# Performance work log

Measured on AMD Instinct MI355X. Metric: run time of the kernel, lower is better.

The kernel has to match this reference:

```python
import jax, jax.numpy as jnp
import numpy as np

ODIM = 8192      # output dim (slice target)
MSIZE = 64       # tile size
N_BLOCKS = 1024  # size of shared block bank


def setup_inputs() -> dict:
    key = jax.random.key(0)
    k1, k2, k3, k4 = jax.random.split(key, 4)
    x = jax.random.normal(k1, (256, 8192), dtype=jnp.float32)
    # bank of msize x msize module blocks (scaled like fan-in init)
    blocks = jax.random.normal(k2, (N_BLOCKS, MSIZE, MSIZE), dtype=jnp.float32) * 0.02
    bound = 1.0 / np.sqrt(ODIM).astype(np.float32)
    bias = jax.random.uniform(k3, (ODIM,), dtype=jnp.float32, minval=-bound, maxval=bound)
    # parts: [icount, ocount] indices into the block bank
    parts = jax.random.randint(k4, (128, 128), 0, N_BLOCKS)
    return {"x": x, "blocks": blocks, "bias": bias, "parts": parts}


def reference(x, blocks, bias, parts):
    icount, ocount = parts.shape
    m = blocks.shape[-1]
    # build_mosaic: gather blocks per parts and tile into a dense weight matrix
    fc = blocks[parts]                                   # [ic, oc, m, m]
    fc_mat = fc.transpose(0, 2, 1, 3).reshape(icount * m, ocount * m)
    # idim (8192) is divisible by msize, so pad is identity (rem == 0 branch)
    y = x @ fc_mat                                       # [B, oc*m]
    y = y[..., :ODIM] + bias                             # slice + bias; post = Identity
    return y
```

## Files before the change

### kernel.cpp

```cpp
#include <hip/hip_runtime.h>
#include <stdint.h>

#define BATCH 256
#define IDIM  8192
#define ODIM  8192
#define MS    64
#define IC    128
#define OC    128
#define NB    1024

#define TM 256
#define TN 256
#define KSPLIT 8
#define NIB (IC / KSPLIT)

typedef __bf16 bf16x8 __attribute__((ext_vector_type(8)));
typedef float  floatx4 __attribute__((ext_vector_type(4)));

#define WAITCNT_VM(n) ((((n) & 15) | (((n) >> 4) << 14)) | 0x70 | 0xF00)

__device__ __forceinline__ void async_load16(unsigned short* lds_p, const unsigned short* g_p) {
    __builtin_amdgcn_global_load_lds(
        (const __attribute__((address_space(1))) unsigned int*)g_p,
        (__attribute__((address_space(3))) unsigned int*)lds_p,
        16, 0, 0);
}

__device__ __forceinline__ unsigned short f32_to_bf16(float f) {
    unsigned int u = __float_as_uint(f);
    u += 0x7FFFu + ((u >> 16) & 1u);
    return (unsigned short)(u >> 16);
}

#define XCONV_BLKS 1024
#define PT_BLKS 64
__global__ void k_convert(const float* __restrict__ x, const float* __restrict__ blocks,
                          const int* __restrict__ parts,
                          unsigned short* __restrict__ xb, unsigned short* __restrict__ bt,
                          int* __restrict__ pT) {
    __shared__ float tile[MS][MS + 1];
    int b = blockIdx.x;
    if (b < NB) {
        const float4* src4 = (const float4*)(blocks + (size_t)b * MS * MS);
        unsigned short* dst = bt + (size_t)b * MS * MS;
        #pragma unroll
        for (int i = 0; i < 4; ++i) {
            int slot = i * 256 + threadIdx.x;
            int r = slot >> 4, c4 = (slot & 15) * 4;
            float4 v = src4[slot];
            tile[r][c4 + 0] = v.x; tile[r][c4 + 1] = v.y;
            tile[r][c4 + 2] = v.z; tile[r][c4 + 3] = v.w;
        }
        __syncthreads();
        #pragma unroll
        for (int i = 0; i < 2; ++i) {
            int slot = i * 256 + threadIdx.x;
            int c = slot >> 3, o = slot & 7;
            union { unsigned short s[8]; uint4 v; } u;
            #pragma unroll
            for (int j = 0; j < 8; ++j) u.s[j] = f32_to_bf16(tile[o * 8 + j][c]);
            *(uint4*)(dst + c * MS + o * 8) = u.v;
        }
    } else if (b < NB + XCONV_BLKS) {
        int t = (b - NB) * 256 + threadIdx.x;
        const float4* x4 = (const float4*)x;
        float4 a = x4[2 * t], bb = x4[2 * t + 1];
        union { unsigned short s[8]; uint4 v; } u;
        u.s[0] = f32_to_bf16(a.x);  u.s[1] = f32_to_bf16(a.y);
        u.s[2] = f32_to_bf16(a.z);  u.s[3] = f32_to_bf16(a.w);
        u.s[4] = f32_to_bf16(bb.x); u.s[5] = f32_to_bf16(bb.y);
        u.s[6] = f32_to_bf16(bb.z); u.s[7] = f32_to_bf16(bb.w);
        ((uint4*)xb)[t] = u.v;
    } else {
        int t = (b - NB - XCONV_BLKS) * 256 + threadIdx.x;
        int oc = t >> 7, ic = t & 127;
        pT[t] = parts[ic * OC + oc];
    }
}

__global__ __launch_bounds__(1024, 1)
void k_mosaic_gemm(const unsigned short* __restrict__ xb,
                   const unsigned short* __restrict__ bt,
                   const int* __restrict__ pT,
                   float* __restrict__ partial) {
    __shared__ __align__(16) unsigned short a_lds[2][TM * MS];
    __shared__ __align__(16) unsigned short b_lds[2][TN * MS];

    const int tid  = threadIdx.x;
    const int lane = tid & 63;
    const int wave = tid >> 6;
    const int wrow = wave >> 2;
    const int wcol = wave & 3;
    const int nt = blockIdx.x;
    const int ks = blockIdx.y;

    const int ob0 = nt * 4;
    const int ib0 = ks * NIB;

    const int row  = lane & 15;
    const int quad = lane >> 4;

    int pv = pT[(ob0 + (lane >> 4)) * IC + ib0 + (lane & 15)];

    int a_off[2][4], b_off[2][4];
    #pragma unroll
    for (int kk = 0; kk < 2; ++kk) {
        int oct = kk * 4 + quad;
        #pragma unroll
        for (int mi = 0; mi < 4; ++mi) {
            int r = wrow * 64 + mi * 16 + row;
            a_off[kk][mi] = r * MS + ((oct ^ (r & 7)) << 3);
        }
        #pragma unroll
        for (int ni = 0; ni < 4; ++ni) {
            int n = wcol * 64 + ni * 16 + row;
            b_off[kk][ni] = n * MS + ((oct ^ (n & 7)) << 3);
        }
    }

    floatx4 acc[4][4];
    #pragma unroll
    for (int mi = 0; mi < 4; ++mi)
        #pragma unroll
        for (int ni = 0; ni < 4; ++ni)
            acc[mi][ni] = (floatx4){0.f, 0.f, 0.f, 0.f};

#define STAGE(buf, ib_, q0, q1, q2, q3) do {                                  \
    _Pragma("unroll")                                                         \
    for (int j = 0; j < 2; ++j) {                                             \
        int slot = j * 1024 + tid;                                            \
        int m = slot >> 3;                                                    \
        int oct = (slot & 7) ^ (m & 7);                                       \
        async_load16(&a_lds[buf][slot * 8],                                   \
                     xb + (size_t)m * IDIM + (ib_) * MS + oct * 8);           \
    }                                                                         \
    _Pragma("unroll")                                                         \
    for (int j = 0; j < 2; ++j) {                                             \
        int slot = j * 1024 + tid;                                            \
        int n = slot >> 3;                                                    \
        int oct = (slot & 7) ^ (n & 7);                                       \
        int p = (j == 0) ? ((tid < 512) ? (q0) : (q1))                        \
                         : ((tid < 512) ? (q2) : (q3));                       \
        async_load16(&b_lds[buf][slot * 8],                                   \
                     bt + (size_t)p * (MS * MS) + (n & 63) * MS + oct * 8);   \
    } } while (0)

#define COMPUTE(buf) do {                                                     \
    _Pragma("unroll")                                                         \
    for (int kk = 0; kk < 2; ++kk) {                                          \
        bf16x8 af[4], bfr[4];                                                 \
        _Pragma("unroll")                                                     \
        for (int mi = 0; mi < 4; ++mi)                                        \
            af[mi] = *(const bf16x8*)&a_lds[buf][a_off[kk][mi]];              \
        _Pragma("unroll")                                                     \
        for (int ni = 0; ni < 4; ++ni)                                        \
            bfr[ni] = *(const bf16x8*)&b_lds[buf][b_off[kk][ni]];             \
        _Pragma("unroll")                                                     \
        for (int mi = 0; mi < 4; ++mi)                                        \
            _Pragma("unroll")                                                 \
            for (int ni = 0; ni < 4; ++ni)                                    \
                acc[mi][ni] = __builtin_amdgcn_mfma_f32_16x16x32_bf16(        \
                    af[mi], bfr[ni], acc[mi][ni], 0, 0, 0);                   \
    } } while (0)

    {
        int q0 = __shfl(pv, 0), q1 = __shfl(pv, 16), q2 = __shfl(pv, 32), q3 = __shfl(pv, 48);
        STAGE(0, ib0 + 0, q0, q1, q2, q3);
    }

    for (int i = 0; i < NIB - 1; ++i) {
        int q0 = __shfl(pv, i + 1),      q1 = __shfl(pv, 16 + i + 1);
        int q2 = __shfl(pv, 32 + i + 1), q3 = __shfl(pv, 48 + i + 1);
        STAGE((i + 1) & 1, ib0 + i + 1, q0, q1, q2, q3);
        __builtin_amdgcn_s_waitcnt(WAITCNT_VM(4));
        __builtin_amdgcn_s_barrier();
        COMPUTE(i & 1);
        __builtin_amdgcn_s_barrier();
    }
    __builtin_amdgcn_s_waitcnt(WAITCNT_VM(0));
    __builtin_amdgcn_s_barrier();
    COMPUTE((NIB - 1) & 1);

    float* out = partial + (size_t)ks * BATCH * ODIM;
    #pragma unroll
    for (int mi = 0; mi < 4; ++mi)
        #pragma unroll
        for (int ni = 0; ni < 4; ++ni)
            #pragma unroll
            for (int r = 0; r < 4; ++r) {
                int rowg = wrow * 64 + mi * 16 + quad * 4 + r;
                int colg = nt * TN + wcol * 64 + ni * 16 + row;
                out[(size_t)rowg * ODIM + colg] = acc[mi][ni][r];
            }
}

__global__ void k_reduce_bias(const float* __restrict__ partial,
                              const float* __restrict__ bias,
                              float* __restrict__ out) {
    int t = blockIdx.x * 256 + threadIdx.x;
    const float4* b4 = (const float4*)bias;
    float4 c = b4[t & (ODIM / 4 - 1)];
    float4 r = {c.x, c.y, c.z, c.w};
    #pragma unroll
    for (int k = 0; k < KSPLIT; ++k) {
        const float4* p = (const float4*)(partial + (size_t)k * BATCH * ODIM);
        float4 a = p[t];
        r.x += a.x; r.y += a.y; r.z += a.z; r.w += a.w;
    }
    ((float4*)out)[t] = r;
}

extern "C" void kernel_launch(void* const* d_in, const int* in_sizes, int n_in,
                              void* d_out, int out_size, void* d_ws, size_t ws_size,
                              hipStream_t stream) {
    const float* x      = (const float*)d_in[0];
    const float* blocks = (const float*)d_in[1];
    const float* bias   = (const float*)d_in[2];
    const int*   parts  = (const int*)d_in[3];
    float* out = (float*)d_out;

    char* ws = (char*)d_ws;
    unsigned short* xb      = (unsigned short*)ws;
    unsigned short* btb     = (unsigned short*)(ws + (4u << 20));
    int*            pTr     = (int*)(ws + (12u << 20));
    float*          partial = (float*)(ws + (13u << 20));

    k_convert<<<NB + XCONV_BLKS + PT_BLKS, 256, 0, stream>>>(x, blocks, parts, xb, btb, pTr);
    k_mosaic_gemm<<<dim3(ODIM / TN, KSPLIT), 1024, 0, stream>>>(xb, btb, pTr, partial);
    k_reduce_bias<<<(BATCH * ODIM) / (256 * 4), 256, 0, stream>>>(partial, bias, out);
}
```

Baseline: 125.5 us.

## Switch GEMM to 256x128 tiles with triple-buffered LDS and split-K of four

After: 118.9 us. 1.06x faster.

```diff
diff --git a/kernel.cpp b/kernel.cpp
--- a/kernel.cpp
+++ b/kernel.cpp
@@ -10,9 +10,12 @@
 #define NB    1024
 
 #define TM 256
-#define TN 256
-#define KSPLIT 8
+#define TN 128
+#define KSPLIT 4
 #define NIB (IC / KSPLIT)
+
+#define STAGE_USH (48 * 1024 / 2)
+#define B_OFF_USH (32 * 1024 / 2)
 
 typedef __bf16 bf16x8 __attribute__((ext_vector_type(8)));
 typedef float  floatx4 __attribute__((ext_vector_type(4)));
@@ -78,29 +81,29 @@
     }
 }
 
-__global__ __launch_bounds__(1024, 1)
+extern __shared__ unsigned short smem[];
+
+__global__ __launch_bounds__(512, 1)
 void k_mosaic_gemm(const unsigned short* __restrict__ xb,
                    const unsigned short* __restrict__ bt,
                    const int* __restrict__ pT,
                    float* __restrict__ partial) {
-    __shared__ __align__(16) unsigned short a_lds[2][TM * MS];
-    __shared__ __align__(16) unsigned short b_lds[2][TN * MS];
-
     const int tid  = threadIdx.x;
     const int lane = tid & 63;
     const int wave = tid >> 6;
-    const int wrow = wave >> 2;
-    const int wcol = wave & 3;
+    const int wrow = wave >> 1;
+    const int wcol = wave & 1;
     const int nt = blockIdx.x;
     const int ks = blockIdx.y;
 
-    const int ob0 = nt * 4;
+    const int ob0 = nt * 2;
     const int ib0 = ks * NIB;
 
     const int row  = lane & 15;
     const int quad = lane >> 4;
 
-    int pv = pT[(ob0 + (lane >> 4)) * IC + ib0 + (lane & 15)];
+    int pv0 = pT[ob0 * IC + ib0 + (lane & 31)];
+    int pv1 = pT[(ob0 + 1) * IC + ib0 + (lane & 31)];
 
     int a_off[2][4], b_off[2][4];
     #pragma unroll
@@ -114,7 +117,7 @@
         #pragma unroll
         for (int ni = 0; ni < 4; ++ni) {
             int n = wcol * 64 + ni * 16 + row;
-            b_off[kk][ni] = n * MS + ((oct ^ (n & 7)) << 3);
+            b_off[kk][ni] = B_OFF_USH + n * MS + ((oct ^ (n & 7)) << 3);
         }
     }
 
@@ -125,36 +128,35 @@
         for (int ni = 0; ni < 4; ++ni)
             acc[mi][ni] = (floatx4){0.f, 0.f, 0.f, 0.f};
 
-#define STAGE(buf, ib_, q0, q1, q2, q3) do {                                  \
+#define STAGE(base, ib_, p0_, p1_) do {                                       \
     _Pragma("unroll")                                                         \
-    for (int j = 0; j < 2; ++j) {                                             \
-        int slot = j * 1024 + tid;                                            \
+    for (int j = 0; j < 4; ++j) {                                             \
+        int slot = j * 512 + tid;               \
         int m = slot >> 3;                                                    \
         int oct = (slot & 7) ^ (m & 7);                                       \
-        async_load16(&a_lds[buf][slot * 8],                                   \
+        async_load16(smem + (base) + slot * 8,                                \
                      xb + (size_t)m * IDIM + (ib_) * MS + oct * 8);           \
     }                                                                         \
     _Pragma("unroll")                                                         \
     for (int j = 0; j < 2; ++j) {                                             \
-        int slot = j * 1024 + tid;                                            \
+        int slot = j * 512 + tid;               \
         int n = slot >> 3;                                                    \
         int oct = (slot & 7) ^ (n & 7);                                       \
-        int p = (j == 0) ? ((tid < 512) ? (q0) : (q1))                        \
-                         : ((tid < 512) ? (q2) : (q3));                       \
-        async_load16(&b_lds[buf][slot * 8],                                   \
+        int p = (j == 0) ? (p0_) : (p1_);                                     \
+        async_load16(smem + (base) + B_OFF_USH + slot * 8,                    \
                      bt + (size_t)p * (MS * MS) + (n & 63) * MS + oct * 8);   \
     } } while (0)
 
-#define COMPUTE(buf) do {                                                     \
+#define COMPUTE(base) do {                                                    \
     _Pragma("unroll")                                                         \
     for (int kk = 0; kk < 2; ++kk) {                                          \
         bf16x8 af[4], bfr[4];                                                 \
         _Pragma("unroll")                                                     \
         for (int mi = 0; mi < 4; ++mi)                                        \
-            af[mi] = *(const bf16x8*)&a_lds[buf][a_off[kk][mi]];              \
+            af[mi] = *(const bf16x8*)(smem + (base) + a_off[kk][mi]);         \
         _Pragma("unroll")                                                     \
         for (int ni = 0; ni < 4; ++ni)                                        \
-            bfr[ni] = *(const bf16x8*)&b_lds[buf][b_off[kk][ni]];             \
+            bfr[ni] = *(const bf16x8*)(smem + (base) + b_off[kk][ni]);        \
         _Pragma("unroll")                                                     \
         for (int mi = 0; mi < 4; ++mi)                                        \
             _Pragma("unroll")                                                 \
@@ -164,22 +166,43 @@
     } } while (0)
 
     {
-        int q0 = __shfl(pv, 0), q1 = __shfl(pv, 16), q2 = __shfl(pv, 32), q3 = __shfl(pv, 48);
-        STAGE(0, ib0 + 0, q0, q1, q2, q3);
-    }
-
-    for (int i = 0; i < NIB - 1; ++i) {
-        int q0 = __shfl(pv, i + 1),      q1 = __shfl(pv, 16 + i + 1);
-        int q2 = __shfl(pv, 32 + i + 1), q3 = __shfl(pv, 48 + i + 1);
-        STAGE((i + 1) & 1, ib0 + i + 1, q0, q1, q2, q3);
-        __builtin_amdgcn_s_waitcnt(WAITCNT_VM(4));
+        int q0 = __shfl(pv0, 0), q1 = __shfl(pv1, 0);
+        STAGE(0, ib0 + 0, q0, q1);
+        q0 = __shfl(pv0, 1); q1 = __shfl(pv1, 1);
+        STAGE(STAGE_USH, ib0 + 1, q0, q1);
+        q0 = __shfl(pv0, 2); q1 = __shfl(pv1, 2);
+        STAGE(2 * STAGE_USH, ib0 + 2, q0, q1);
+    }
+
+    int base = 0;
+    for (int i = 0; i < NIB - 3; ++i) {
+        __builtin_amdgcn_sched_barrier(0);
+        __builtin_amdgcn_s_waitcnt(WAITCNT_VM(12));
         __builtin_amdgcn_s_barrier();
-        COMPUTE(i & 1);
+        COMPUTE(base);
         __builtin_amdgcn_s_barrier();
-    }
+        int q0 = __shfl(pv0, i + 3), q1 = __shfl(pv1, i + 3);
+        STAGE(base, ib0 + i + 3, q0, q1);
+        base = (base == 2 * STAGE_USH) ? 0 : base + STAGE_USH;
+    }
+    __builtin_amdgcn_sched_barrier(0);
+    __builtin_amdgcn_s_waitcnt(WAITCNT_VM(12));
+    __builtin_amdgcn_s_barrier();
+    COMPUTE(base);
+    __builtin_amdgcn_s_barrier();
+    base = (base == 2 * STAGE_USH) ? 0 : base + STAGE_USH;
+
+    __builtin_amdgcn_sched_barrier(0);
+    __builtin_amdgcn_s_waitcnt(WAITCNT_VM(6));
+    __builtin_amdgcn_s_barrier();
+    COMPUTE(base);
+    __builtin_amdgcn_s_barrier();
+    base = (base == 2 * STAGE_USH) ? 0 : base + STAGE_USH;
+
+    __builtin_amdgcn_sched_barrier(0);
     __builtin_amdgcn_s_waitcnt(WAITCNT_VM(0));
     __builtin_amdgcn_s_barrier();
-    COMPUTE((NIB - 1) & 1);
+    COMPUTE(base);
 
     float* out = partial + (size_t)ks * BATCH * ODIM;
     #pragma unroll
@@ -225,7 +248,14 @@
     int*            pTr     = (int*)(ws + (12u << 20));
     float*          partial = (float*)(ws + (13u << 20));
 
+    static bool attr_set = false;
+    if (!attr_set) {
+        hipFuncSetAttribute((const void*)k_mosaic_gemm,
+                            hipFuncAttributeMaxDynamicSharedMemorySize, 3 * 48 * 1024);
+        attr_set = true;
+    }
+
     k_convert<<<NB + XCONV_BLKS + PT_BLKS, 256, 0, stream>>>(x, blocks, parts, xb, btb, pTr);
-    k_mosaic_gemm<<<dim3(ODIM / TN, KSPLIT), 1024, 0, stream>>>(xb, btb, pTr, partial);
+    k_mosaic_gemm<<<dim3(ODIM / TN, KSPLIT), 512, 3 * 48 * 1024, stream>>>(xb, btb, pTr, partial);
     k_reduce_bias<<<(BATCH * ODIM) / (256 * 4), 256, 0, stream>>>(partial, bias, out);
 }
```
